# Kernel tuning notes

Hardware: AMD Instinct MI355X
Metric: run time of the kernel (lower is better)

Reference implementation:

```python
import jax, jax.numpy as jnp
import numpy as np

N = 50000        # nodes
E = 800000       # edges
D_IN = 128       # input_dim
HID = 64         # hidden_dim (out_channels per head)
HEADS = 2
OUT = 64         # output_dim
NEG_GAT = 0.2    # GAT leaky_relu slope
NEG_ACT = 0.01   # F.leaky_relu default slope between layers


def _segment_softmax(s, dst, n):
    # softmax over edges grouped by destination node, per (head, channel)
    m = jax.ops.segment_max(s, dst, num_segments=n)          # [N,H,C]
    e = jnp.exp(s - m[dst])                                  # [E,H,C]
    z = jax.ops.segment_sum(e, dst, num_segments=n)          # [N,H,C]
    return e / z[dst]


def _gat_layer(x, W, b, att_l, att_r, src, dst):
    H, C = att_l.shape
    h = (x @ W.T + b).reshape(-1, H, C)                      # lin_l == lin_r (shared)
    al = att_l[None] * h                                     # [N,H,C]
    ar = att_r[None] * h
    s = jax.nn.leaky_relu(al[src] + ar[dst], NEG_GAT)        # [E,H,C]
    alpha = _segment_softmax(s, dst, N)
    out = jax.ops.segment_sum(h[src] * alpha, dst, num_segments=N)
    return out.reshape(-1, H * C)


def setup_inputs() -> dict:
    key = jax.random.key(0)
    ks = jax.random.split(key, 16)
    HC = HEADS * HID
    sc = lambda fan: 1.0 / np.sqrt(fan)
    return {
        "emb_weight": jax.random.normal(ks[0], (N, D_IN), jnp.float32),
        "edge_index": jax.random.randint(ks[1], (2, E), 0, N, jnp.int32),
        # GAT layer 0: in=D_IN
        "W0": jax.random.normal(ks[2], (HC, D_IN), jnp.float32) * sc(D_IN),
        "b0": jnp.zeros((HC,), jnp.float32),
        "attl0": jax.random.normal(ks[3], (HEADS, HID), jnp.float32) * sc(HID),
        "attr0": jax.random.normal(ks[4], (HEADS, HID), jnp.float32) * sc(HID),
        # GAT layer 1: in=HEADS*HID
        "W1": jax.random.normal(ks[5], (HC, HC), jnp.float32) * sc(HC),
        "b1": jnp.zeros((HC,), jnp.float32),
        "attl1": jax.random.normal(ks[6], (HEADS, HID), jnp.float32) * sc(HID),
        "attr1": jax.random.normal(ks[7], (HEADS, HID), jnp.float32) * sc(HID),
        # post_mp: Linear(HC, HID) -> Linear(HID, OUT)
        "pW1": jax.random.normal(ks[8], (HID, HC), jnp.float32) * sc(HC),
        "pb1": jnp.zeros((HID,), jnp.float32),
        "pW2": jax.random.normal(ks[9], (OUT, HID), jnp.float32) * sc(HID),
        "pb2": jnp.zeros((OUT,), jnp.float32),
    }


def reference(emb_weight, edge_index, W0, b0, attl0, attr0, W1, b1, attl1, attr1,
              pW1, pb1, pW2, pb2):
    src, dst = edge_index[0], edge_index[1]
    x = _gat_layer(emb_weight, W0, b0, attl0, attr0, src, dst)
    x = jax.nn.leaky_relu(x, NEG_ACT)
    x = _gat_layer(x, W1, b1, attl1, attr1, src, dst)
    x = jax.nn.leaky_relu(x, NEG_ACT)
    x = x @ pW1.T + pb1
    x = x @ pW2.T + pb2                                      # [N, OUT]
    u = x[src]
    v = x[dst]
    sig = jax.nn.sigmoid(jnp.sum(u * v, axis=-1))            # [E]
    return (sig, x)
```

## Files before the change

kernel.cpp:

```cpp
#include <hip/hip_runtime.h>
#include <hip/hip_bf16.h>
#include <hip/hip_fp16.h>
#include <math.h>

#define N_NODES 50000
#define N_EDGES 800000
#define HC      128
#define OUTD    64
#define NBKT    ((N_NODES + 63) / 64)

#if defined(__has_builtin)
#if __has_builtin(__builtin_amdgcn_exp2f)
#define EXP2(x) __builtin_amdgcn_exp2f(x)
#endif
#endif
#ifndef EXP2
#define EXP2(x) __expf((x) * 0.69314718055994531f)
#endif

typedef _Float16 f16x8 __attribute__((ext_vector_type(8)));
typedef float f32x4 __attribute__((ext_vector_type(4)));


__global__ __launch_bounds__(1024) void k_hist(const int* __restrict__ dst,
                                               int* __restrict__ bcnt, int e_cnt) {
    __shared__ int lh[NBKT];
    for (int i = threadIdx.x; i < NBKT; i += 1024) lh[i] = 0;
    __syncthreads();
    int base = blockIdx.x * 8192;
    for (int i = threadIdx.x; i < 8192; i += 1024) {
        int e = base + i;
        if (e < e_cnt) atomicAdd(&lh[dst[e] >> 6], 1);
    }
    __syncthreads();
    for (int i = threadIdx.x; i < NBKT; i += 1024) {
        int c = lh[i];
        if (c) atomicAdd(&bcnt[i], c);
    }
}

__global__ __launch_bounds__(1024) void k_bscan(const int* __restrict__ bcnt,
                                                int* __restrict__ bbase,
                                                int* __restrict__ bcur) {
    __shared__ int wsum[16];
    __shared__ int wexc[16];
    int t = threadIdx.x, lane = t & 63, wid = t >> 6;
    int v = (t < NBKT) ? bcnt[t] : 0;
    int incl = v;
    #pragma unroll
    for (int s = 1; s < 64; s <<= 1) {
        int u = __shfl_up(incl, s, 64);
        if (lane >= s) incl += u;
    }
    if (lane == 63) wsum[wid] = incl;
    __syncthreads();
    if (wid == 0 && lane < 16) {
        int w = wsum[lane];
        int wi = w;
        #pragma unroll
        for (int s = 1; s < 16; s <<= 1) {
            int u = __shfl_up(wi, s, 64);
            if (lane >= s) wi += u;
        }
        wexc[lane] = wi - w;
    }
    __syncthreads();
    int ex = wexc[wid] + incl - v;
    if (t < NBKT) { bbase[t] = ex; bcur[t] = ex; }
    if (t == NBKT - 1) bbase[NBKT] = ex + v;
}

__global__ __launch_bounds__(1024) void k_bscatter(const int* __restrict__ src,
                                                   const int* __restrict__ dst,
                                                   int* __restrict__ bcur,
                                                   uint2* __restrict__ ebuf, int e_cnt) {
    __shared__ int lcnt[NBKT];
    __shared__ int lbase[NBKT];
    for (int i = threadIdx.x; i < NBKT; i += 1024) lcnt[i] = 0;
    __syncthreads();
    int base = blockIdx.x * 8192;
    int myS[8], myD[8], myR[8];
    #pragma unroll
    for (int j = 0; j < 8; ++j) {
        int e = base + threadIdx.x + j * 1024;
        if (e < e_cnt) {
            myS[j] = src[e];
            myD[j] = dst[e];
            myR[j] = atomicAdd(&lcnt[myD[j] >> 6], 1);
        } else myD[j] = -1;
    }
    __syncthreads();
    for (int i = threadIdx.x; i < NBKT; i += 1024) {
        int c = lcnt[i];
        lbase[i] = c ? atomicAdd(&bcur[i], c) : 0;
    }
    __syncthreads();
    #pragma unroll
    for (int j = 0; j < 8; ++j) {
        if (myD[j] >= 0) {
            int bkt = myD[j] >> 6;
            ebuf[lbase[bkt] + myR[j]] =
                make_uint2((unsigned)myS[j], (unsigned)myD[j]);
        }
    }
}

__global__ __launch_bounds__(256) void k_bfinal(const uint2* __restrict__ ebuf,
                                                const int* __restrict__ bbase,
                                                int* __restrict__ off,
                                                int* __restrict__ esrc, int n) {
    __shared__ int ncnt[64];
    __shared__ int ncur[64];
    int b = blockIdx.x;
    int t = threadIdx.x;
    int ebeg = bbase[b], eend = bbase[b + 1];
    if (t < 64) ncnt[t] = 0;
    __syncthreads();
    for (int e = ebeg + t; e < eend; e += 256)
        atomicAdd(&ncnt[ebuf[e].y & 63], 1);
    __syncthreads();
    if (t < 64) {
        int v = ncnt[t];
        int incl = v;
        #pragma unroll
        for (int s = 1; s < 64; s <<= 1) {
            int u = __shfl_up(incl, s, 64);
            if (t >= s) incl += u;
        }
        int ex = incl - v;
        ncur[t] = ex;
        int node = b * 64 + t;
        if (node <= n) off[node] = ebeg + ex;
    }
    __syncthreads();
    for (int e = ebeg + t; e < eend; e += 256) {
        uint2 ed = ebuf[e];
        int r = atomicAdd(&ncur[ed.y & 63], 1);
        esrc[ebeg + r] = (int)ed.x;
    }
}


__global__ void k_prep(const float* __restrict__ W0, const float* __restrict__ W1,
                       const float* __restrict__ pW1, const float* __restrict__ pb1,
                       const float* __restrict__ pW2, const float* __restrict__ pb2,
                       __half* __restrict__ Wh0, __half* __restrict__ Wh1,
                       float* __restrict__ Wct, float* __restrict__ bc) {
    int i = blockIdx.x * blockDim.x + threadIdx.x;
    if (i < HC * HC) {
        Wh0[i] = __float2half(W0[i]);
        Wh1[i] = __float2half(W1[i]);
    } else if (i < HC * HC + HC * OUTD) {
        int j = i - HC * HC;
        int k = j >> 6, o2 = j & 63;
        float s = 0.f;
        for (int m = 0; m < 64; ++m) s += pW2[o2 * 64 + m] * pW1[m * 128 + k];
        Wct[k * 64 + o2] = s;
    } else if (i < HC * HC + HC * OUTD + OUTD) {
        int o2 = i - HC * HC - HC * OUTD;
        float s = pb2[o2];
        for (int m = 0; m < 64; ++m) s += pW2[o2 * 64 + m] * pb1[m];
        bc[o2] = s;
    }
}


#define LSTR 136

__global__ __launch_bounds__(256) void k_lin128(const float* __restrict__ x,
                                                const __half* __restrict__ Wh,
                                                const float* __restrict__ bias,
                                                __half* __restrict__ h, int n) {
    __shared__ _Float16 wsh[128 * LSTR];
    __shared__ _Float16 xsh[32 * LSTR];
    int t = threadIdx.x;
    int node0 = blockIdx.x * 32;
    for (int i = t; i < 2048; i += 256) {
        int r = i >> 4, c16 = i & 15;
        *(uint4*)&wsh[r * LSTR + c16 * 8] = ((const uint4*)Wh)[i];
    }
    for (int i = t; i < 1024; i += 256) {
        int r = i >> 5, c4 = i & 31;
        int gn = node0 + r;
        float4 v = (gn < n) ? ((const float4*)x)[(size_t)gn * 32 + c4]
                            : make_float4(0.f, 0.f, 0.f, 0.f);
        union { _Float16 hh[4]; uint2 u; } cv;
        cv.hh[0] = (_Float16)v.x; cv.hh[1] = (_Float16)v.y;
        cv.hh[2] = (_Float16)v.z; cv.hh[3] = (_Float16)v.w;
        *(uint2*)&xsh[r * LSTR + c4 * 4] = cv.u;
    }
    __syncthreads();
    int w = t >> 6, l = t & 63;
    int lr = l & 15, lg = l >> 4;
    int nrow0 = (w >> 1) * 16;
    int ccol0 = (w & 1) * 64;
    f32x4 acc0 = {0.f, 0.f, 0.f, 0.f};
    f32x4 acc1 = acc0, acc2 = acc0, acc3 = acc0;
    #pragma unroll
    for (int kk = 0; kk < 4; ++kk) {
        int ko = kk * 32 + lg * 8;
        f16x8 a  = *(const f16x8*)&xsh[(nrow0 + lr) * LSTR + ko];
        f16x8 b0 = *(const f16x8*)&wsh[(ccol0 +  0 + lr) * LSTR + ko];
        f16x8 b1 = *(const f16x8*)&wsh[(ccol0 + 16 + lr) * LSTR + ko];
        f16x8 b2 = *(const f16x8*)&wsh[(ccol0 + 32 + lr) * LSTR + ko];
        f16x8 b3 = *(const f16x8*)&wsh[(ccol0 + 48 + lr) * LSTR + ko];
        acc0 = __builtin_amdgcn_mfma_f32_16x16x32_f16(a, b0, acc0, 0, 0, 0);
        acc1 = __builtin_amdgcn_mfma_f32_16x16x32_f16(a, b1, acc1, 0, 0, 0);
        acc2 = __builtin_amdgcn_mfma_f32_16x16x32_f16(a, b2, acc2, 0, 0, 0);
        acc3 = __builtin_amdgcn_mfma_f32_16x16x32_f16(a, b3, acc3, 0, 0, 0);
    }
    float b0v = bias[ccol0 +  0 + lr];
    float b1v = bias[ccol0 + 16 + lr];
    float b2v = bias[ccol0 + 32 + lr];
    float b3v = bias[ccol0 + 48 + lr];
    __syncthreads();
    int orow = nrow0 + lg * 4;
    #pragma unroll
    for (int j = 0; j < 4; ++j) {
        xsh[(orow + j) * LSTR + ccol0 +  0 + lr] = (_Float16)(acc0[j] + b0v);
        xsh[(orow + j) * LSTR + ccol0 + 16 + lr] = (_Float16)(acc1[j] + b1v);
        xsh[(orow + j) * LSTR + ccol0 + 32 + lr] = (_Float16)(acc2[j] + b2v);
        xsh[(orow + j) * LSTR + ccol0 + 48 + lr] = (_Float16)(acc3[j] + b3v);
    }
    __syncthreads();
    for (int i = t; i < 1024; i += 256) {
        int r = i >> 5, c4 = i & 31;
        int gn = node0 + r;
        if (gn < n)
            *(uint2*)&h[(size_t)gn * 128 + c4 * 4] = *(uint2*)&xsh[r * LSTR + c4 * 4];
    }
}


__global__ __launch_bounds__(256) void k_gat_agg(const __half* __restrict__ h,
                                                 const int* __restrict__ off,
                                                 const int* __restrict__ esrc,
                                                 const float* __restrict__ attl,
                                                 const float* __restrict__ attr,
                                                 float* __restrict__ xout, int n,
                                                 float neg_out) {
    const float L2E = 1.4426950408889634f;
    int wid  = threadIdx.x >> 6;
    int lane = threadIdx.x & 63;
    int node = blockIdx.x * 4 + wid;
    if (node >= n) return;
    int half = lane >> 5;
    int cq   = lane & 31;
    uint32_t cq8 = (uint32_t)cq << 3;

    const char* hb = (const char*)h;

    float4 alv = ((const float4*)attl)[cq];
    float4 arv = ((const float4*)attr)[cq];
    uint2 hdr = *(const uint2*)(hb + ((((uint32_t)node << 8)) | cq8));
    float2 hd01 = __half22float2(((const __half2*)&hdr)[0]);
    float2 hd23 = __half22float2(((const __half2*)&hdr)[1]);
    float al0 = alv.x * L2E, al1 = alv.y * L2E;
    float al2 = alv.z * L2E, al3 = alv.w * L2E;
    float ar0 = arv.x * hd01.x * L2E, ar1 = arv.y * hd01.y * L2E;
    float ar2 = arv.z * hd23.x * L2E, ar3 = arv.w * hd23.y * L2E;

    float z0 = 0.f, z1 = 0.f, z2 = 0.f, z3 = 0.f;
    float a0 = 0.f, a1 = 0.f, a2 = 0.f, a3 = 0.f;

    int beg = off[node], end = off[node + 1];

#define STEP(sAv)                                                              \
    {   uint32_t voff = (((uint32_t)(sAv)) << 8) | cq8;                        \
        uint2 hv = *(const uint2*)(hb + voff);                                 \
        float2 f01 = __half22float2(((const __half2*)&hv)[0]);                 \
        float2 f23 = __half22float2(((const __half2*)&hv)[1]);                 \
        float t0 = fmaf(al0, f01.x, ar0), t1 = fmaf(al1, f01.y, ar1);          \
        float t2 = fmaf(al2, f23.x, ar2), t3 = fmaf(al3, f23.y, ar3);          \
        float e0 = EXP2(fmaxf(t0, 0.2f * t0)), e1 = EXP2(fmaxf(t1, 0.2f * t1));\
        float e2 = EXP2(fmaxf(t2, 0.2f * t2)), e3 = EXP2(fmaxf(t3, 0.2f * t3));\
        z0 += e0; z1 += e1; z2 += e2; z3 += e3;                                \
        a0 = fmaf(e0, f01.x, a0); a1 = fmaf(e1, f01.y, a1);                    \
        a2 = fmaf(e2, f23.x, a2); a3 = fmaf(e3, f23.y, a3);                    \
    }

    {
        int e = beg;
        #pragma unroll 4
        for (; e + 2 <= end; e += 2) {
            int sA = esrc[e + half];
            STEP(sA);
        }
        if (e < end) {
            int sA = esrc[end - 1];
            if (half == 0) STEP(sA);
        }
    }
#undef STEP

    float zs = z0 + z1 + z2 + z3;
    bool bad = !(zs < 3.0e38f);
    if (beg < end)
        bad = bad || !((z0 > 0.f) && (z1 > 0.f) && (z2 > 0.f) && (z3 > 0.f));

    if (__any(bad)) {
        float m0 = -1e30f, m1 = -1e30f, m2 = -1e30f, m3 = -1e30f;
        for (int e = beg; e < end; ++e) {
            int sA = esrc[e];
            uint2 hv = *(const uint2*)(hb + (((uint32_t)sA << 8) | cq8));
            float2 f01 = __half22float2(((const __half2*)&hv)[0]);
            float2 f23 = __half22float2(((const __half2*)&hv)[1]);
            float t0 = fmaf(al0, f01.x, ar0), t1 = fmaf(al1, f01.y, ar1);
            float t2 = fmaf(al2, f23.x, ar2), t3 = fmaf(al3, f23.y, ar3);
            m0 = fmaxf(m0, fmaxf(t0, 0.2f * t0));
            m1 = fmaxf(m1, fmaxf(t1, 0.2f * t1));
            m2 = fmaxf(m2, fmaxf(t2, 0.2f * t2));
            m3 = fmaxf(m3, fmaxf(t3, 0.2f * t3));
        }
        z0 = z1 = z2 = z3 = 0.f;
        a0 = a1 = a2 = a3 = 0.f;
        for (int e = beg; e < end; ++e) {
            int sA = esrc[e];
            uint2 hv = *(const uint2*)(hb + (((uint32_t)sA << 8) | cq8));
            float2 f01 = __half22float2(((const __half2*)&hv)[0]);
            float2 f23 = __half22float2(((const __half2*)&hv)[1]);
            float t0 = fmaf(al0, f01.x, ar0), t1 = fmaf(al1, f01.y, ar1);
            float t2 = fmaf(al2, f23.x, ar2), t3 = fmaf(al3, f23.y, ar3);
            float e0 = EXP2(fmaxf(t0, 0.2f * t0) - m0);
            float e1 = EXP2(fmaxf(t1, 0.2f * t1) - m1);
            float e2 = EXP2(fmaxf(t2, 0.2f * t2) - m2);
            float e3 = EXP2(fmaxf(t3, 0.2f * t3) - m3);
            z0 += e0; z1 += e1; z2 += e2; z3 += e3;
            a0 = fmaf(e0, f01.x, a0); a1 = fmaf(e1, f01.y, a1);
            a2 = fmaf(e2, f23.x, a2); a3 = fmaf(e3, f23.y, a3);
        }
    } else {
        z0 += __shfl_xor(z0, 32, 64); z1 += __shfl_xor(z1, 32, 64);
        z2 += __shfl_xor(z2, 32, 64); z3 += __shfl_xor(z3, 32, 64);
        a0 += __shfl_xor(a0, 32, 64); a1 += __shfl_xor(a1, 32, 64);
        a2 += __shfl_xor(a2, 32, 64); a3 += __shfl_xor(a3, 32, 64);
    }

    if (half == 0) {
        float o0 = (z0 > 0.f) ? a0 / z0 : 0.f;
        float o1 = (z1 > 0.f) ? a1 / z1 : 0.f;
        float o2 = (z2 > 0.f) ? a2 / z2 : 0.f;
        float o3 = (z3 > 0.f) ? a3 / z3 : 0.f;
        o0 = fmaxf(o0, neg_out * o0);
        o1 = fmaxf(o1, neg_out * o1);
        o2 = fmaxf(o2, neg_out * o2);
        o3 = fmaxf(o3, neg_out * o3);
        *(float4*)&xout[(size_t)node * 128 + cq * 4] = make_float4(o0, o1, o2, o3);
    }
}


#define FMA4(acc, wv, sv)                                                      \
    acc.x = fmaf(wv.x, sv, acc.x); acc.y = fmaf(wv.y, sv, acc.y);              \
    acc.z = fmaf(wv.z, sv, acc.z); acc.w = fmaf(wv.w, sv, acc.w);

__global__ __launch_bounds__(256) void k_lin64(const float* __restrict__ x,
                                               const float* __restrict__ Wct,
                                               const float* __restrict__ bc,
                                               float* __restrict__ y,
                                               __half* __restrict__ yh, int n) {
    __shared__ float ws[64 * 64];
    __shared__ float xs[16 * 128];
    int t = threadIdx.x;
    int node0 = blockIdx.x * 16;
    for (int i = t; i < 512; i += 256) {
        int row = i >> 5, c = i & 31;
        int gn = node0 + row;
        ((float4*)xs)[i] = (gn < n) ? ((const float4*)x)[(size_t)gn * 32 + c]
                                    : make_float4(0.f, 0.f, 0.f, 0.f);
    }
    int l = t & 15;
    int g = t >> 4;
    float4 acc = ((const float4*)bc)[l];
    const float4* xr = (const float4*)&xs[g * 128];

    for (int chunk = 0; chunk < 2; ++chunk) {
        __syncthreads();
        const float4* wsrc = (const float4*)&Wct[chunk * 64 * 64];
        for (int i = t; i < 1024; i += 256)
            ((float4*)ws)[i] = wsrc[i];
        __syncthreads();
        int kb = chunk * 16;
        #pragma unroll 4
        for (int k4 = 0; k4 < 16; ++k4) {
            float4 xv = xr[kb + k4];
            const float* wr = &ws[k4 * 256];
            float4 w0 = ((const float4*)&wr[0])[l];
            float4 w1 = ((const float4*)&wr[64])[l];
            float4 w2 = ((const float4*)&wr[128])[l];
            float4 w3 = ((const float4*)&wr[192])[l];
            FMA4(acc, w0, xv.x); FMA4(acc, w1, xv.y);
            FMA4(acc, w2, xv.z); FMA4(acc, w3, xv.w);
        }
    }

    int gn = node0 + g;
    if (gn < n) {
        ((float4*)&y[(size_t)gn * 64])[l] = acc;
        union { __half2 h2[2]; uint2 u; } p;
        p.h2[0] = __floats2half2_rn(acc.x, acc.y);
        p.h2[1] = __floats2half2_rn(acc.z, acc.w);
        *(uint2*)&yh[(size_t)gn * 64 + l * 4] = p.u;
    }
}


__global__ __launch_bounds__(256) void k_edge_score(const __half* __restrict__ xh,
                                                    const int* __restrict__ src,
                                                    const int* __restrict__ dst,
                                                    float* __restrict__ out, int e_cnt) {
    int t = blockIdx.x * 256 + threadIdx.x;
    int e = t >> 3;
    int l = t & 7;
    if (e >= e_cnt) return;
    int u = src[e], v = dst[e];
    uint4 ua = ((const uint4*)&xh[(size_t)u * 64])[l];
    uint4 vb = ((const uint4*)&xh[(size_t)v * 64])[l];
    const __half2* pa = (const __half2*)&ua;
    const __half2* pb = (const __half2*)&vb;
    float d = 0.f;
    #pragma unroll
    for (int j = 0; j < 4; ++j) {
        float2 fa = __half22float2(pa[j]);
        float2 fb = __half22float2(pb[j]);
        d = fmaf(fa.x, fb.x, d);
        d = fmaf(fa.y, fb.y, d);
    }
    d += __shfl_xor(d, 1);
    d += __shfl_xor(d, 2);
    d += __shfl_xor(d, 4);
    if (l == 0) out[e] = 1.f / (1.f + __expf(-d));
}


extern "C" void kernel_launch(void* const* d_in, const int* in_sizes, int n_in,
                              void* d_out, int out_size, void* d_ws, size_t ws_size,
                              hipStream_t stream) {
    const float* emb   = (const float*)d_in[0];
    const int*   ei    = (const int*)d_in[1];
    const float* W0    = (const float*)d_in[2];
    const float* b0    = (const float*)d_in[3];
    const float* attl0 = (const float*)d_in[4];
    const float* attr0 = (const float*)d_in[5];
    const float* W1    = (const float*)d_in[6];
    const float* b1    = (const float*)d_in[7];
    const float* attl1 = (const float*)d_in[8];
    const float* attr1 = (const float*)d_in[9];
    const float* pW1   = (const float*)d_in[10];
    const float* pb1   = (const float*)d_in[11];
    const float* pW2   = (const float*)d_in[12];
    const float* pb2   = (const float*)d_in[13];

    const int* src = ei;
    const int* dst = ei + N_EDGES;

    float* out = (float*)d_out;
    float* xo  = out + N_EDGES;

    char* ws = (char*)d_ws;
    size_t o = 0;
    auto alloc = [&](size_t bytes) {
        char* p = ws + o;
        o = (o + bytes + 255) & ~(size_t)255;
        return p;
    };
    int*    off   = (int*)alloc((size_t)(N_NODES + 1) * 4);
    int*    esrc  = (int*)alloc((size_t)N_EDGES * 4);
    int*    bcnt  = (int*)alloc((size_t)(NBKT + 1) * 4);
    int*    bbase = (int*)alloc((size_t)(NBKT + 1) * 4);
    int*    bcur  = (int*)alloc((size_t)(NBKT + 1) * 4);
    uint2*  ebuf  = (uint2*)alloc((size_t)N_EDGES * 8);
    __half* hbuf  = (__half*)alloc((size_t)N_NODES * HC * 2);
    float*  xbuf  = (float*)alloc((size_t)N_NODES * HC * 4);
    __half* yh    = (__half*)alloc((size_t)N_NODES * OUTD * 2);
    __half* Wh0   = (__half*)alloc((size_t)HC * HC * 2);
    __half* Wh1   = (__half*)alloc((size_t)HC * HC * 2);
    float*  Wct   = (float*)alloc((size_t)HC * OUTD * 4);
    float*  bc    = (float*)alloc((size_t)OUTD * 4);
    (void)ws_size; (void)in_sizes; (void)n_in; (void)out_size;

    const int L128_NB = (N_NODES + 31) / 32;
    const int L64_NB  = (N_NODES + 15) / 16;
    const int EB_NB   = (N_EDGES + 8191) / 8192;
    const int PREP_N  = HC * HC + HC * OUTD + OUTD;

    k_prep<<<(PREP_N + 255) / 256, 256, 0, stream>>>(W0, W1, pW1, pb1, pW2, pb2,
                                                     Wh0, Wh1, Wct, bc);

    hipMemsetAsync(bcnt, 0, (size_t)(NBKT + 1) * 4, stream);
    k_hist    <<<EB_NB, 1024, 0, stream>>>(dst, bcnt, N_EDGES);
    k_bscan   <<<1, 1024, 0, stream>>>(bcnt, bbase, bcur);
    k_bscatter<<<EB_NB, 1024, 0, stream>>>(src, dst, bcur, ebuf, N_EDGES);
    k_bfinal  <<<NBKT, 256, 0, stream>>>(ebuf, bbase, off, esrc, N_NODES);

    k_lin128<<<L128_NB, 256, 0, stream>>>(emb, Wh0, b0, hbuf, N_NODES);
    k_gat_agg<<<(N_NODES + 3) / 4, 256, 0, stream>>>(hbuf, off, esrc, attl0, attr0,
                                                     xbuf, N_NODES, 0.01f);
    k_lin128<<<L128_NB, 256, 0, stream>>>(xbuf, Wh1, b1, hbuf, N_NODES);
    k_gat_agg<<<(N_NODES + 3) / 4, 256, 0, stream>>>(hbuf, off, esrc, attl1, attr1,
                                                     xbuf, N_NODES, 0.01f);

    k_lin64<<<L64_NB, 256, 0, stream>>>(xbuf, Wct, bc, xo, yh, N_NODES);

    k_edge_score<<<(N_EDGES * 8 + 255) / 256, 256, 0, stream>>>(yh, src, dst, out, N_EDGES);
}
```

Before: 193.4 us.

## Process four edges per wave in GAT aggregation and use MFMA for final linear

The GAT aggregation kernel now splits each wave into four 16-lane groups. Each lane loads 16-byte chunks covering 8 channels and four edges are handled in parallel, with partial sums merged by cross-lane shuffles before the fallback check. This reduces the number of serial iterations per node and widens the memory loads. The final folded 128→64 linear is rewritten to use fp16 MFMA 16x16x32 with weights and activations staged in LDS as half precision, tiling 64 nodes per block. This adds fp16 rounding of the layer input and doubles the per-lane register accumulators in the aggregation.

```diff
diff --git a/kernel.cpp b/kernel.cpp
--- a/kernel.cpp
+++ b/kernel.cpp
@@ -145,7 +145,7 @@
                        const float* __restrict__ pW1, const float* __restrict__ pb1,
                        const float* __restrict__ pW2, const float* __restrict__ pb2,
                        __half* __restrict__ Wh0, __half* __restrict__ Wh1,
-                       float* __restrict__ Wct, float* __restrict__ bc) {
+                       __half* __restrict__ Wcht, float* __restrict__ bc) {
     int i = blockIdx.x * blockDim.x + threadIdx.x;
     if (i < HC * HC) {
         Wh0[i] = __float2half(W0[i]);
@@ -155,7 +155,7 @@
         int k = j >> 6, o2 = j & 63;
         float s = 0.f;
         for (int m = 0; m < 64; ++m) s += pW2[o2 * 64 + m] * pW1[m * 128 + k];
-        Wct[k * 64 + o2] = s;
+        Wcht[o2 * 128 + k] = __float2half(s);
     } else if (i < HC * HC + HC * OUTD + OUTD) {
         int o2 = i - HC * HC - HC * OUTD;
         float s = pb2[o2];
@@ -244,163 +244,216 @@
     int lane = threadIdx.x & 63;
     int node = blockIdx.x * 4 + wid;
     if (node >= n) return;
-    int half = lane >> 5;
-    int cq   = lane & 31;
-    uint32_t cq8 = (uint32_t)cq << 3;
+    int q  = lane >> 4;
+    int cs = lane & 15;
+    uint32_t cs16 = (uint32_t)cs << 4;
 
     const char* hb = (const char*)h;
 
-    float4 alv = ((const float4*)attl)[cq];
-    float4 arv = ((const float4*)attr)[cq];
-    uint2 hdr = *(const uint2*)(hb + ((((uint32_t)node << 8)) | cq8));
-    float2 hd01 = __half22float2(((const __half2*)&hdr)[0]);
-    float2 hd23 = __half22float2(((const __half2*)&hdr)[1]);
-    float al0 = alv.x * L2E, al1 = alv.y * L2E;
-    float al2 = alv.z * L2E, al3 = alv.w * L2E;
-    float ar0 = arv.x * hd01.x * L2E, ar1 = arv.y * hd01.y * L2E;
-    float ar2 = arv.z * hd23.x * L2E, ar3 = arv.w * hd23.y * L2E;
+    float4 alv0 = ((const float4*)attl)[cs * 2];
+    float4 alv1 = ((const float4*)attl)[cs * 2 + 1];
+    float4 arv0 = ((const float4*)attr)[cs * 2];
+    float4 arv1 = ((const float4*)attr)[cs * 2 + 1];
+    uint4 hdr = *(const uint4*)(hb + ((((uint32_t)node << 8)) | cs16));
+    const __half2* pd = (const __half2*)&hdr;
+    float2 d01 = __half22float2(pd[0]), d23 = __half22float2(pd[1]);
+    float2 d45 = __half22float2(pd[2]), d67 = __half22float2(pd[3]);
+    float al0 = alv0.x * L2E, al1 = alv0.y * L2E, al2 = alv0.z * L2E, al3 = alv0.w * L2E;
+    float al4 = alv1.x * L2E, al5 = alv1.y * L2E, al6 = alv1.z * L2E, al7 = alv1.w * L2E;
+    float ar0 = arv0.x * d01.x * L2E, ar1 = arv0.y * d01.y * L2E;
+    float ar2 = arv0.z * d23.x * L2E, ar3 = arv0.w * d23.y * L2E;
+    float ar4 = arv1.x * d45.x * L2E, ar5 = arv1.y * d45.y * L2E;
+    float ar6 = arv1.z * d67.x * L2E, ar7 = arv1.w * d67.y * L2E;
 
     float z0 = 0.f, z1 = 0.f, z2 = 0.f, z3 = 0.f;
+    float z4 = 0.f, z5 = 0.f, z6 = 0.f, z7 = 0.f;
     float a0 = 0.f, a1 = 0.f, a2 = 0.f, a3 = 0.f;
+    float a4 = 0.f, a5 = 0.f, a6 = 0.f, a7 = 0.f;
 
     int beg = off[node], end = off[node + 1];
 
 #define STEP(sAv)                                                              \
-    {   uint32_t voff = (((uint32_t)(sAv)) << 8) | cq8;                        \
-        uint2 hv = *(const uint2*)(hb + voff);                                 \
-        float2 f01 = __half22float2(((const __half2*)&hv)[0]);                 \
-        float2 f23 = __half22float2(((const __half2*)&hv)[1]);                 \
+    {   uint4 hv = *(const uint4*)(hb + ((((uint32_t)(sAv)) << 8) | cs16));    \
+        const __half2* pf = (const __half2*)&hv;                               \
+        float2 f01 = __half22float2(pf[0]), f23 = __half22float2(pf[1]);       \
+        float2 f45 = __half22float2(pf[2]), f67 = __half22float2(pf[3]);       \
         float t0 = fmaf(al0, f01.x, ar0), t1 = fmaf(al1, f01.y, ar1);          \
         float t2 = fmaf(al2, f23.x, ar2), t3 = fmaf(al3, f23.y, ar3);          \
+        float t4 = fmaf(al4, f45.x, ar4), t5 = fmaf(al5, f45.y, ar5);          \
+        float t6 = fmaf(al6, f67.x, ar6), t7 = fmaf(al7, f67.y, ar7);          \
         float e0 = EXP2(fmaxf(t0, 0.2f * t0)), e1 = EXP2(fmaxf(t1, 0.2f * t1));\
         float e2 = EXP2(fmaxf(t2, 0.2f * t2)), e3 = EXP2(fmaxf(t3, 0.2f * t3));\
+        float e4 = EXP2(fmaxf(t4, 0.2f * t4)), e5 = EXP2(fmaxf(t5, 0.2f * t5));\
+        float e6 = EXP2(fmaxf(t6, 0.2f * t6)), e7 = EXP2(fmaxf(t7, 0.2f * t7));\
         z0 += e0; z1 += e1; z2 += e2; z3 += e3;                                \
+        z4 += e4; z5 += e5; z6 += e6; z7 += e7;                                \
         a0 = fmaf(e0, f01.x, a0); a1 = fmaf(e1, f01.y, a1);                    \
         a2 = fmaf(e2, f23.x, a2); a3 = fmaf(e3, f23.y, a3);                    \
+        a4 = fmaf(e4, f45.x, a4); a5 = fmaf(e5, f45.y, a5);                    \
+        a6 = fmaf(e6, f67.x, a6); a7 = fmaf(e7, f67.y, a7);                    \
     }
 
     {
         int e = beg;
-        #pragma unroll 4
-        for (; e + 2 <= end; e += 2) {
-            int sA = esrc[e + half];
+        #pragma unroll 2
+        for (; e + 4 <= end; e += 4) {
+            int sA = esrc[e + q];
             STEP(sA);
         }
-        if (e < end) {
-            int sA = esrc[end - 1];
-            if (half == 0) STEP(sA);
+        int r = end - e;
+        if (r > 0) {
+            int sA = (q < r) ? esrc[e + q] : 0;
+            if (q < r) STEP(sA);
         }
     }
 #undef STEP
 
-    float zs = z0 + z1 + z2 + z3;
+#define MRG(v) v += __shfl_xor(v, 16, 64); v += __shfl_xor(v, 32, 64);
+    MRG(z0) MRG(z1) MRG(z2) MRG(z3) MRG(z4) MRG(z5) MRG(z6) MRG(z7)
+    MRG(a0) MRG(a1) MRG(a2) MRG(a3) MRG(a4) MRG(a5) MRG(a6) MRG(a7)
+#undef MRG
+
+    float zs = (z0 + z1 + z2 + z3) + (z4 + z5 + z6 + z7);
     bool bad = !(zs < 3.0e38f);
     if (beg < end)
-        bad = bad || !((z0 > 0.f) && (z1 > 0.f) && (z2 > 0.f) && (z3 > 0.f));
+        bad = bad || !((z0 > 0.f) && (z1 > 0.f) && (z2 > 0.f) && (z3 > 0.f) &&
+                       (z4 > 0.f) && (z5 > 0.f) && (z6 > 0.f) && (z7 > 0.f));
 
     if (__any(bad)) {
         float m0 = -1e30f, m1 = -1e30f, m2 = -1e30f, m3 = -1e30f;
+        float m4 = -1e30f, m5 = -1e30f, m6 = -1e30f, m7 = -1e30f;
         for (int e = beg; e < end; ++e) {
             int sA = esrc[e];
-            uint2 hv = *(const uint2*)(hb + (((uint32_t)sA << 8) | cq8));
-            float2 f01 = __half22float2(((const __half2*)&hv)[0]);
-            float2 f23 = __half22float2(((const __half2*)&hv)[1]);
+            uint4 hv = *(const uint4*)(hb + (((uint32_t)sA << 8) | cs16));
+            const __half2* pf = (const __half2*)&hv;
+            float2 f01 = __half22float2(pf[0]), f23 = __half22float2(pf[1]);
+            float2 f45 = __half22float2(pf[2]), f67 = __half22float2(pf[3]);
             float t0 = fmaf(al0, f01.x, ar0), t1 = fmaf(al1, f01.y, ar1);
             float t2 = fmaf(al2, f23.x, ar2), t3 = fmaf(al3, f23.y, ar3);
-            m0 = fmaxf(m0, fmaxf(t0, 0.2f * t0));
-            m1 = fmaxf(m1, fmaxf(t1, 0.2f * t1));
-            m2 = fmaxf(m2, fmaxf(t2, 0.2f * t2));
-            m3 = fmaxf(m3, fmaxf(t3, 0.2f * t3));
-        }
-        z0 = z1 = z2 = z3 = 0.f;
-        a0 = a1 = a2 = a3 = 0.f;
+            float t4 = fmaf(al4, f45.x, ar4), t5 = fmaf(al5, f45.y, ar5);
+            float t6 = fmaf(al6, f67.x, ar6), t7 = fmaf(al7, f67.y, ar7);
+            m0 = fmaxf(m0, fmaxf(t0, 0.2f * t0)); m1 = fmaxf(m1, fmaxf(t1, 0.2f * t1));
+            m2 = fmaxf(m2, fmaxf(t2, 0.2f * t2)); m3 = fmaxf(m3, fmaxf(t3, 0.2f * t3));
+            m4 = fmaxf(m4, fmaxf(t4, 0.2f * t4)); m5 = fmaxf(m5, fmaxf(t5, 0.2f * t5));
+            m6 = fmaxf(m6, fmaxf(t6, 0.2f * t6)); m7 = fmaxf(m7, fmaxf(t7, 0.2f * t7));
+        }
+        z0 = z1 = z2 = z3 = z4 = z5 = z6 = z7 = 0.f;
+        a0 = a1 = a2 = a3 = a4 = a5 = a6 = a7 = 0.f;
         for (int e = beg; e < end; ++e) {
             int sA = esrc[e];
-            uint2 hv = *(const uint2*)(hb + (((uint32_t)sA << 8) | cq8));
-            float2 f01 = __half22float2(((const __half2*)&hv)[0]);
-            float2 f23 = __half22float2(((const __half2*)&hv)[1]);
+            uint4 hv = *(const uint4*)(hb + (((uint32_t)sA << 8) | cs16));
+            const __half2* pf = (const __half2*)&hv;
+            float2 f01 = __half22float2(pf[0]), f23 = __half22float2(pf[1]);
+            float2 f45 = __half22float2(pf[2]), f67 = __half22float2(pf[3]);
             float t0 = fmaf(al0, f01.x, ar0), t1 = fmaf(al1, f01.y, ar1);
             float t2 = fmaf(al2, f23.x, ar2), t3 = fmaf(al3, f23.y, ar3);
-            float e0 = EXP2(fmaxf(t0, 0.2f * t0) - m0);
-            float e1 = EXP2(fmaxf(t1, 0.2f * t1) - m1);
-            float e2 = EXP2(fmaxf(t2, 0.2f * t2) - m2);
-            float e3 = EXP2(fmaxf(t3, 0.2f * t3) - m3);
+            float t4 = fmaf(al4, f45.x, ar4), t5 = fmaf(al5, f45.y, ar5);
+            float t6 = fmaf(al6, f67.x, ar6), t7 = fmaf(al7, f67.y, ar7);
+            float e0 = EXP2(fmaxf(t0, 0.2f * t0) - m0), e1 = EXP2(fmaxf(t1, 0.2f * t1) - m1);
+            float e2 = EXP2(fmaxf(t2, 0.2f * t2) - m2), e3 = EXP2(fmaxf(t3, 0.2f * t3) - m3);
+            float e4 = EXP2(fmaxf(t4, 0.2f * t4) - m4), e5 = EXP2(fmaxf(t5, 0.2f * t5) - m5);
+            float e6 = EXP2(fmaxf(t6, 0.2f * t6) - m6), e7 = EXP2(fmaxf(t7, 0.2f * t7) - m7);
             z0 += e0; z1 += e1; z2 += e2; z3 += e3;
+            z4 += e4; z5 += e5; z6 += e6; z7 += e7;
             a0 = fmaf(e0, f01.x, a0); a1 = fmaf(e1, f01.y, a1);
             a2 = fmaf(e2, f23.x, a2); a3 = fmaf(e3, f23.y, a3);
-        }
-    } else {
-        z0 += __shfl_xor(z0, 32, 64); z1 += __shfl_xor(z1, 32, 64);
-        z2 += __shfl_xor(z2, 32, 64); z3 += __shfl_xor(z3, 32, 64);
-        a0 += __shfl_xor(a0, 32, 64); a1 += __shfl_xor(a1, 32, 64);
-        a2 += __shfl_xor(a2, 32, 64); a3 += __shfl_xor(a3, 32, 64);
-    }
-
-    if (half == 0) {
+            a4 = fmaf(e4, f45.x, a4); a5 = fmaf(e5, f45.y, a5);
+            a6 = fmaf(e6, f67.x, a6); a7 = fmaf(e7, f67.y, a7);
+        }
+    }
+
+    if (q == 0) {
         float o0 = (z0 > 0.f) ? a0 / z0 : 0.f;
         float o1 = (z1 > 0.f) ? a1 / z1 : 0.f;
         float o2 = (z2 > 0.f) ? a2 / z2 : 0.f;
         float o3 = (z3 > 0.f) ? a3 / z3 : 0.f;
-        o0 = fmaxf(o0, neg_out * o0);
-        o1 = fmaxf(o1, neg_out * o1);
-        o2 = fmaxf(o2, neg_out * o2);
-        o3 = fmaxf(o3, neg_out * o3);
-        *(float4*)&xout[(size_t)node * 128 + cq * 4] = make_float4(o0, o1, o2, o3);
-    }
-}
-
-
-#define FMA4(acc, wv, sv)                                                      \
-    acc.x = fmaf(wv.x, sv, acc.x); acc.y = fmaf(wv.y, sv, acc.y);              \
-    acc.z = fmaf(wv.z, sv, acc.z); acc.w = fmaf(wv.w, sv, acc.w);
+        float o4 = (z4 > 0.f) ? a4 / z4 : 0.f;
+        float o5 = (z5 > 0.f) ? a5 / z5 : 0.f;
+        float o6 = (z6 > 0.f) ? a6 / z6 : 0.f;
+        float o7 = (z7 > 0.f) ? a7 / z7 : 0.f;
+        o0 = fmaxf(o0, neg_out * o0); o1 = fmaxf(o1, neg_out * o1);
+        o2 = fmaxf(o2, neg_out * o2); o3 = fmaxf(o3, neg_out * o3);
+        o4 = fmaxf(o4, neg_out * o4); o5 = fmaxf(o5, neg_out * o5);
+        o6 = fmaxf(o6, neg_out * o6); o7 = fmaxf(o7, neg_out * o7);
+        float* op = &xout[(size_t)node * 128 + cs * 8];
+        *(float4*)&op[0] = make_float4(o0, o1, o2, o3);
+        *(float4*)&op[4] = make_float4(o4, o5, o6, o7);
+    }
+}
+
 
 __global__ __launch_bounds__(256) void k_lin64(const float* __restrict__ x,
-                                               const float* __restrict__ Wct,
+                                               const __half* __restrict__ Wcht,
                                                const float* __restrict__ bc,
                                                float* __restrict__ y,
                                                __half* __restrict__ yh, int n) {
-    __shared__ float ws[64 * 64];
-    __shared__ float xs[16 * 128];
+    __shared__ _Float16 wsh[64 * LSTR];
+    __shared__ _Float16 xsh[64 * LSTR];
     int t = threadIdx.x;
-    int node0 = blockIdx.x * 16;
-    for (int i = t; i < 512; i += 256) {
-        int row = i >> 5, c = i & 31;
-        int gn = node0 + row;
-        ((float4*)xs)[i] = (gn < n) ? ((const float4*)x)[(size_t)gn * 32 + c]
-                                    : make_float4(0.f, 0.f, 0.f, 0.f);
-    }
-    int l = t & 15;
-    int g = t >> 4;
-    float4 acc = ((const float4*)bc)[l];
-    const float4* xr = (const float4*)&xs[g * 128];
-
-    for (int chunk = 0; chunk < 2; ++chunk) {
-        __syncthreads();
-        const float4* wsrc = (const float4*)&Wct[chunk * 64 * 64];
-        for (int i = t; i < 1024; i += 256)
-            ((float4*)ws)[i] = wsrc[i];
-        __syncthreads();
-        int kb = chunk * 16;
-        #pragma unroll 4
-        for (int k4 = 0; k4 < 16; ++k4) {
-            float4 xv = xr[kb + k4];
-            const float* wr = &ws[k4 * 256];
-            float4 w0 = ((const float4*)&wr[0])[l];
-            float4 w1 = ((const float4*)&wr[64])[l];
-            float4 w2 = ((const float4*)&wr[128])[l];
-            float4 w3 = ((const float4*)&wr[192])[l];
-            FMA4(acc, w0, xv.x); FMA4(acc, w1, xv.y);
-            FMA4(acc, w2, xv.z); FMA4(acc, w3, xv.w);
-        }
-    }
-
-    int gn = node0 + g;
-    if (gn < n) {
-        ((float4*)&y[(size_t)gn * 64])[l] = acc;
-        union { __half2 h2[2]; uint2 u; } p;
-        p.h2[0] = __floats2half2_rn(acc.x, acc.y);
-        p.h2[1] = __floats2half2_rn(acc.z, acc.w);
-        *(uint2*)&yh[(size_t)gn * 64 + l * 4] = p.u;
+    int node0 = blockIdx.x * 64;
+    for (int i = t; i < 1024; i += 256) {
+        int r = i >> 4, c16 = i & 15;
+        *(uint4*)&wsh[r * LSTR + c16 * 8] = ((const uint4*)Wcht)[i];
+    }
+    for (int i = t; i < 2048; i += 256) {
+        int r = i >> 5, c4 = i & 31;
+        int gn = node0 + r;
+        float4 v = (gn < n) ? ((const float4*)x)[(size_t)gn * 32 + c4]
+                            : make_float4(0.f, 0.f, 0.f, 0.f);
+        union { _Float16 hh[4]; uint2 u; } cv;
+        cv.hh[0] = (_Float16)v.x; cv.hh[1] = (_Float16)v.y;
+        cv.hh[2] = (_Float16)v.z; cv.hh[3] = (_Float16)v.w;
+        *(uint2*)&xsh[r * LSTR + c4 * 4] = cv.u;
+    }
+    __syncthreads();
+    int w = t >> 6, l = t & 63;
+    int lr = l & 15, lg = l >> 4;
+    int nrow0 = w * 16;
+    f32x4 acc0 = {0.f, 0.f, 0.f, 0.f};
+    f32x4 acc1 = acc0, acc2 = acc0, acc3 = acc0;
+    #pragma unroll
+    for (int kk = 0; kk < 4; ++kk) {
+        int ko = kk * 32 + lg * 8;
+        f16x8 a  = *(const f16x8*)&xsh[(nrow0 + lr) * LSTR + ko];
+        f16x8 b0 = *(const f16x8*)&wsh[( 0 + lr) * LSTR + ko];
+        f16x8 b1 = *(const f16x8*)&wsh[(16 + lr) * LSTR + ko];
+        f16x8 b2 = *(const f16x8*)&wsh[(32 + lr) * LSTR + ko];
+        f16x8 b3 = *(const f16x8*)&wsh[(48 + lr) * LSTR + ko];
+        acc0 = __builtin_amdgcn_mfma_f32_16x16x32_f16(a, b0, acc0, 0, 0, 0);
+        acc1 = __builtin_amdgcn_mfma_f32_16x16x32_f16(a, b1, acc1, 0, 0, 0);
+        acc2 = __builtin_amdgcn_mfma_f32_16x16x32_f16(a, b2, acc2, 0, 0, 0);
+        acc3 = __builtin_amdgcn_mfma_f32_16x16x32_f16(a, b3, acc3, 0, 0, 0);
+    }
+    float b0v = bc[ 0 + lr], b1v = bc[16 + lr];
+    float b2v = bc[32 + lr], b3v = bc[48 + lr];
+    __syncthreads();
+    float* osh = (float*)wsh;
+    int orow = nrow0 + lg * 4;
+    #pragma unroll
+    for (int j = 0; j < 4; ++j) {
+        float v0 = acc0[j] + b0v, v1 = acc1[j] + b1v;
+        float v2 = acc2[j] + b2v, v3 = acc3[j] + b3v;
+        osh[(orow + j) * 68 +  0 + lr] = v0;
+        osh[(orow + j) * 68 + 16 + lr] = v1;
+        osh[(orow + j) * 68 + 32 + lr] = v2;
+        osh[(orow + j) * 68 + 48 + lr] = v3;
+        xsh[(orow + j) * LSTR +  0 + lr] = (_Float16)v0;
+        xsh[(orow + j) * LSTR + 16 + lr] = (_Float16)v1;
+        xsh[(orow + j) * LSTR + 32 + lr] = (_Float16)v2;
+        xsh[(orow + j) * LSTR + 48 + lr] = (_Float16)v3;
+    }
+    __syncthreads();
+    for (int i = t; i < 1024; i += 256) {
+        int r = i >> 4, c4 = i & 15;
+        int gn = node0 + r;
+        if (gn < n)
+            ((float4*)&y[(size_t)gn * 64])[c4] = *(float4*)&osh[r * 68 + c4 * 4];
+    }
+    for (int i = t; i < 1024; i += 256) {
+        int r = i >> 4, c4 = i & 15;
+        int gn = node0 + r;
+        if (gn < n)
+            *(uint2*)&yh[(size_t)gn * 64 + c4 * 4] = *(uint2*)&xsh[r * LSTR + c4 * 4];
     }
 }
 
@@ -475,17 +528,17 @@
     __half* yh    = (__half*)alloc((size_t)N_NODES * OUTD * 2);
     __half* Wh0   = (__half*)alloc((size_t)HC * HC * 2);
     __half* Wh1   = (__half*)alloc((size_t)HC * HC * 2);
-    float*  Wct   = (float*)alloc((size_t)HC * OUTD * 4);
+    __half* Wcht  = (__half*)alloc((size_t)HC * OUTD * 2);
     float*  bc    = (float*)alloc((size_t)OUTD * 4);
     (void)ws_size; (void)in_sizes; (void)n_in; (void)out_size;
 
     const int L128_NB = (N_NODES + 31) / 32;
-    const int L64_NB  = (N_NODES + 15) / 16;
+    const int L64_NB  = (N_NODES + 63) / 64;
     const int EB_NB   = (N_EDGES + 8191) / 8192;
     const int PREP_N  = HC * HC + HC * OUTD + OUTD;
 
     k_prep<<<(PREP_N + 255) / 256, 256, 0, stream>>>(W0, W1, pW1, pb1, pW2, pb2,
-                                                     Wh0, Wh1, Wct, bc);
+                                                     Wh0, Wh1, Wcht, bc);
 
     hipMemsetAsync(bcnt, 0, (size_t)(NBKT + 1) * 4, stream);
     k_hist    <<<EB_NB, 1024, 0, stream>>>(dst, bcnt, N_EDGES);
@@ -500,7 +553,7 @@
     k_gat_agg<<<(N_NODES + 3) / 4, 256, 0, stream>>>(hbuf, off, esrc, attl1, attr1,
                                                      xbuf, N_NODES, 0.01f);
 
-    k_lin64<<<L64_NB, 256, 0, stream>>>(xbuf, Wct, bc, xo, yh, N_NODES);
+    k_lin64<<<L64_NB, 256, 0, stream>>>(xbuf, Wcht, bc, xo, yh, N_NODES);
 
     k_edge_score<<<(N_EDGES * 8 + 255) / 256, 256, 0, stream>>>(yh, src, dst, out, N_EDGES);
 }
```

After: 196.1 us. Within noise of the previous version (+1.4%).

## Use fp16 MFMA for fused post-MP linear kernel with 64-node tiles

Applied to the files above, without the earlier changes.

Rewrites the final 128->64 linear layer to convert activations and the combined weight to fp16 and compute with 16x16x32 MFMA instructions instead of scalar fp32 FMAs. Each block now handles 64 nodes, the weight is stored transposed in fp16, and outputs are staged through shared memory for coalesced fp32 and fp16 stores. This targets the ALU cost and repeated weight loading of the old kernel, at the cost of reduced precision in the fp32 output x.

```diff
diff --git a/kernel.cpp b/kernel.cpp
--- a/kernel.cpp
+++ b/kernel.cpp
@@ -145,7 +145,7 @@
                        const float* __restrict__ pW1, const float* __restrict__ pb1,
                        const float* __restrict__ pW2, const float* __restrict__ pb2,
                        __half* __restrict__ Wh0, __half* __restrict__ Wh1,
-                       float* __restrict__ Wct, float* __restrict__ bc) {
+                       __half* __restrict__ Wcht, float* __restrict__ bc) {
     int i = blockIdx.x * blockDim.x + threadIdx.x;
     if (i < HC * HC) {
         Wh0[i] = __float2half(W0[i]);
@@ -155,7 +155,7 @@
         int k = j >> 6, o2 = j & 63;
         float s = 0.f;
         for (int m = 0; m < 64; ++m) s += pW2[o2 * 64 + m] * pW1[m * 128 + k];
-        Wct[k * 64 + o2] = s;
+        Wcht[o2 * 128 + k] = __float2half(s);
     } else if (i < HC * HC + HC * OUTD + OUTD) {
         int o2 = i - HC * HC - HC * OUTD;
         float s = pb2[o2];
@@ -350,57 +350,78 @@
 }
 
 
-#define FMA4(acc, wv, sv)                                                      \
-    acc.x = fmaf(wv.x, sv, acc.x); acc.y = fmaf(wv.y, sv, acc.y);              \
-    acc.z = fmaf(wv.z, sv, acc.z); acc.w = fmaf(wv.w, sv, acc.w);
-
 __global__ __launch_bounds__(256) void k_lin64(const float* __restrict__ x,
-                                               const float* __restrict__ Wct,
+                                               const __half* __restrict__ Wcht,
                                                const float* __restrict__ bc,
                                                float* __restrict__ y,
                                                __half* __restrict__ yh, int n) {
-    __shared__ float ws[64 * 64];
-    __shared__ float xs[16 * 128];
+    __shared__ _Float16 wsh[64 * LSTR];
+    __shared__ _Float16 xsh[64 * LSTR];
     int t = threadIdx.x;
-    int node0 = blockIdx.x * 16;
-    for (int i = t; i < 512; i += 256) {
-        int row = i >> 5, c = i & 31;
-        int gn = node0 + row;
-        ((float4*)xs)[i] = (gn < n) ? ((const float4*)x)[(size_t)gn * 32 + c]
-                                    : make_float4(0.f, 0.f, 0.f, 0.f);
-    }
-    int l = t & 15;
-    int g = t >> 4;
-    float4 acc = ((const float4*)bc)[l];
-    const float4* xr = (const float4*)&xs[g * 128];
-
-    for (int chunk = 0; chunk < 2; ++chunk) {
-        __syncthreads();
-        const float4* wsrc = (const float4*)&Wct[chunk * 64 * 64];
-        for (int i = t; i < 1024; i += 256)
-            ((float4*)ws)[i] = wsrc[i];
-        __syncthreads();
-        int kb = chunk * 16;
-        #pragma unroll 4
-        for (int k4 = 0; k4 < 16; ++k4) {
-            float4 xv = xr[kb + k4];
-            const float* wr = &ws[k4 * 256];
-            float4 w0 = ((const float4*)&wr[0])[l];
-            float4 w1 = ((const float4*)&wr[64])[l];
-            float4 w2 = ((const float4*)&wr[128])[l];
-            float4 w3 = ((const float4*)&wr[192])[l];
-            FMA4(acc, w0, xv.x); FMA4(acc, w1, xv.y);
-            FMA4(acc, w2, xv.z); FMA4(acc, w3, xv.w);
-        }
-    }
-
-    int gn = node0 + g;
-    if (gn < n) {
-        ((float4*)&y[(size_t)gn * 64])[l] = acc;
-        union { __half2 h2[2]; uint2 u; } p;
-        p.h2[0] = __floats2half2_rn(acc.x, acc.y);
-        p.h2[1] = __floats2half2_rn(acc.z, acc.w);
-        *(uint2*)&yh[(size_t)gn * 64 + l * 4] = p.u;
+    int node0 = blockIdx.x * 64;
+    for (int i = t; i < 1024; i += 256) {
+        int r = i >> 4, c16 = i & 15;
+        *(uint4*)&wsh[r * LSTR + c16 * 8] = ((const uint4*)Wcht)[i];
+    }
+    for (int i = t; i < 2048; i += 256) {
+        int r = i >> 5, c4 = i & 31;
+        int gn = node0 + r;
+        float4 v = (gn < n) ? ((const float4*)x)[(size_t)gn * 32 + c4]
+                            : make_float4(0.f, 0.f, 0.f, 0.f);
+        union { _Float16 hh[4]; uint2 u; } cv;
+        cv.hh[0] = (_Float16)v.x; cv.hh[1] = (_Float16)v.y;
+        cv.hh[2] = (_Float16)v.z; cv.hh[3] = (_Float16)v.w;
+        *(uint2*)&xsh[r * LSTR + c4 * 4] = cv.u;
+    }
+    __syncthreads();
+    int w = t >> 6, l = t & 63;
+    int lr = l & 15, lg = l >> 4;
+    int nrow0 = w * 16;
+    f32x4 acc0 = {0.f, 0.f, 0.f, 0.f};
+    f32x4 acc1 = acc0, acc2 = acc0, acc3 = acc0;
+    #pragma unroll
+    for (int kk = 0; kk < 4; ++kk) {
+        int ko = kk * 32 + lg * 8;
+        f16x8 a  = *(const f16x8*)&xsh[(nrow0 + lr) * LSTR + ko];
+        f16x8 b0 = *(const f16x8*)&wsh[( 0 + lr) * LSTR + ko];
+        f16x8 b1 = *(const f16x8*)&wsh[(16 + lr) * LSTR + ko];
+        f16x8 b2 = *(const f16x8*)&wsh[(32 + lr) * LSTR + ko];
+        f16x8 b3 = *(const f16x8*)&wsh[(48 + lr) * LSTR + ko];
+        acc0 = __builtin_amdgcn_mfma_f32_16x16x32_f16(a, b0, acc0, 0, 0, 0);
+        acc1 = __builtin_amdgcn_mfma_f32_16x16x32_f16(a, b1, acc1, 0, 0, 0);
+        acc2 = __builtin_amdgcn_mfma_f32_16x16x32_f16(a, b2, acc2, 0, 0, 0);
+        acc3 = __builtin_amdgcn_mfma_f32_16x16x32_f16(a, b3, acc3, 0, 0, 0);
+    }
+    float b0v = bc[ 0 + lr], b1v = bc[16 + lr];
+    float b2v = bc[32 + lr], b3v = bc[48 + lr];
+    __syncthreads();
+    float* osh = (float*)wsh;
+    int orow = nrow0 + lg * 4;
+    #pragma unroll
+    for (int j = 0; j < 4; ++j) {
+        float v0 = acc0[j] + b0v, v1 = acc1[j] + b1v;
+        float v2 = acc2[j] + b2v, v3 = acc3[j] + b3v;
+        osh[(orow + j) * 68 +  0 + lr] = v0;
+        osh[(orow + j) * 68 + 16 + lr] = v1;
+        osh[(orow + j) * 68 + 32 + lr] = v2;
+        osh[(orow + j) * 68 + 48 + lr] = v3;
+        xsh[(orow + j) * LSTR +  0 + lr] = (_Float16)v0;
+        xsh[(orow + j) * LSTR + 16 + lr] = (_Float16)v1;
+        xsh[(orow + j) * LSTR + 32 + lr] = (_Float16)v2;
+        xsh[(orow + j) * LSTR + 48 + lr] = (_Float16)v3;
+    }
+    __syncthreads();
+    for (int i = t; i < 1024; i += 256) {
+        int r = i >> 4, c4 = i & 15;
+        int gn = node0 + r;
+        if (gn < n)
+            ((float4*)&y[(size_t)gn * 64])[c4] = *(float4*)&osh[r * 68 + c4 * 4];
+    }
+    for (int i = t; i < 1024; i += 256) {
+        int r = i >> 4, c4 = i & 15;
+        int gn = node0 + r;
+        if (gn < n)
+            *(uint2*)&yh[(size_t)gn * 64 + c4 * 4] = *(uint2*)&xsh[r * LSTR + c4 * 4];
     }
 }
 
@@ -475,17 +496,17 @@
     __half* yh    = (__half*)alloc((size_t)N_NODES * OUTD * 2);
     __half* Wh0   = (__half*)alloc((size_t)HC * HC * 2);
     __half* Wh1   = (__half*)alloc((size_t)HC * HC * 2);
-    float*  Wct   = (float*)alloc((size_t)HC * OUTD * 4);
+    __half* Wcht  = (__half*)alloc((size_t)HC * OUTD * 2);
     float*  bc    = (float*)alloc((size_t)OUTD * 4);
     (void)ws_size; (void)in_sizes; (void)n_in; (void)out_size;
 
     const int L128_NB = (N_NODES + 31) / 32;
-    const int L64_NB  = (N_NODES + 15) / 16;
+    const int L64_NB  = (N_NODES + 63) / 64;
     const int EB_NB   = (N_EDGES + 8191) / 8192;
     const int PREP_N  = HC * HC + HC * OUTD + OUTD;
 
     k_prep<<<(PREP_N + 255) / 256, 256, 0, stream>>>(W0, W1, pW1, pb1, pW2, pb2,
-                                                     Wh0, Wh1, Wct, bc);
+                                                     Wh0, Wh1, Wcht, bc);
 
     hipMemsetAsync(bcnt, 0, (size_t)(NBKT + 1) * 4, stream);
     k_hist    <<<EB_NB, 1024, 0, stream>>>(dst, bcnt, N_EDGES);
@@ -500,7 +521,7 @@
     k_gat_agg<<<(N_NODES + 3) / 4, 256, 0, stream>>>(hbuf, off, esrc, attl1, attr1,
                                                      xbuf, N_NODES, 0.01f);
 
-    k_lin64<<<L64_NB, 256, 0, stream>>>(xbuf, Wct, bc, xo, yh, N_NODES);
+    k_lin64<<<L64_NB, 256, 0, stream>>>(xbuf, Wcht, bc, xo, yh, N_NODES);
 
     k_edge_score<<<(N_EDGES * 8 + 255) / 256, 256, 0, stream>>>(yh, src, dst, out, N_EDGES);
 }
```

New measurement: 179.4 us (median of 2 runs). 1.08x faster.
